# Kernel tuning notes

Measured on AMD Instinct MI355X. Metric: run time of the kernel, lower is better.

The kernel has to match this reference:

```python
import jax, jax.numpy as jnp
import numpy as np

TEMPERATURE = 0.2
HYPER_GAMMA = 0.5
EPS = 1e-12  # torch F.normalize / cosine_similarity eps guard (1e-12 / 1e-8)

def setup_inputs() -> dict:
    key = jax.random.key(0)
    k1, k2 = jax.random.split(key)
    B, D = 4096, 1024
    return {
        "emb_i": jax.random.normal(k1, (B, D), dtype=jnp.float32),
        "emb_j": jax.random.normal(k2, (B, D), dtype=jnp.float32),
    }

def _l2_normalize(x, eps=EPS):
    n = jnp.sqrt(jnp.sum(x * x, axis=1, keepdims=True))
    return x / jnp.maximum(n, eps)

def reference(emb_i, emb_j):
    B = emb_i.shape[0]
    z_i = _l2_normalize(emb_i)
    z_j = _l2_normalize(emb_j)
    # cosine similarity of unit vectors == dot product; sim[a, b] = <z_j[a], z_i[b]>
    sim = jnp.einsum('ad,bd->ab', z_j, z_i)  # [B, B]
    sim_positive = jnp.diagonal(sim)
    positives_exp = jnp.exp(-sim_positive + TEMPERATURE)
    neg_mask = 1.0 - jnp.eye(B, dtype=sim.dtype)
    negatives_exp = neg_mask * jnp.exp(sim - TEMPERATURE)
    positives_sum = jnp.sum(jnp.log1p(positives_exp)) / B
    negatives_sum = jnp.sum(jnp.log1p(negatives_exp)) / (B * (B - 1))
    return HYPER_GAMMA * positives_sum + (1.0 - HYPER_GAMMA) * negatives_sum
```

## Files before the change

kernel.cpp:

```cpp
#include <hip/hip_runtime.h>
#include <math.h>

#define B_ROWS 4096
#define D_DIM  1024
static constexpr float TEMP = 0.2f;
static constexpr float FP8_SCALE = 16.0f;
static constexpr float INV_S2 = 1.0f / 256.0f;

typedef __attribute__((ext_vector_type(4))) float f32x4;

__device__ inline unsigned char f2fp8(float f) {
    unsigned int u = __float_as_uint(f);
    unsigned int s = (u >> 24) & 0x80u;
    float af = fabsf(f);
    unsigned char b;
    if (af >= 0x1.0p-6f) {
        unsigned int au = u & 0x7fffffffu;
        unsigned int lsb = (au >> 20) & 1u;
        au += 0x7ffffu + lsb;
        int e = (int)(au >> 23) - 127 + 7;
        unsigned int m = (au >> 20) & 7u;
        if (e > 15 || (e == 15 && m > 6)) b = 0x7e;
        else b = (unsigned char)((e << 3) | m);
    } else {
        int q = (int)rintf(af * 512.0f);
        b = (unsigned char)(q >= 8 ? 0x08 : q);
    }
    return (unsigned char)(b | s);
}

__device__ inline unsigned int f2fp8x4(float4 v) {
    return (unsigned int)f2fp8(v.x)
         | ((unsigned int)f2fp8(v.y) << 8)
         | ((unsigned int)f2fp8(v.z) << 16)
         | ((unsigned int)f2fp8(v.w) << 24);
}

__device__ inline void gload_lds16(const unsigned char* g, unsigned char* l) {
    __builtin_amdgcn_global_load_lds(
        (const __attribute__((address_space(1))) unsigned int*)g,
        (__attribute__((address_space(3))) unsigned int*)l,
        16, 0, 0);
}


__global__ __launch_bounds__(256) void norm_cast_kernel(
        const float* __restrict__ emb_i, const float* __restrict__ emb_j,
        unsigned char* __restrict__ Zi8, unsigned char* __restrict__ Zj8,
        float* __restrict__ w) {
    const int tid = threadIdx.x;
    if (blockIdx.x == 0 && tid == 0) {
        w[0] = 0.0f; w[1] = 0.0f;
        ((unsigned int*)w)[2] = 0u;
    }
    const int wave = tid >> 6, lane = tid & 63;
    const int row = blockIdx.x * 4 + wave;
    const float* src; unsigned char* dst; int r;
    if (row < B_ROWS) { src = emb_i; dst = Zi8; r = row; }
    else              { src = emb_j; dst = Zj8; r = row - B_ROWS; }

    const float4* p = (const float4*)(src + (size_t)r * D_DIM);
    float4 v0 = p[lane], v1 = p[64 + lane], v2 = p[128 + lane], v3 = p[192 + lane];
    float s = v0.x*v0.x + v0.y*v0.y + v0.z*v0.z + v0.w*v0.w
            + v1.x*v1.x + v1.y*v1.y + v1.z*v1.z + v1.w*v1.w
            + v2.x*v2.x + v2.y*v2.y + v2.z*v2.z + v2.w*v2.w
            + v3.x*v3.x + v3.y*v3.y + v3.z*v3.z + v3.w*v3.w;
    #pragma unroll
    for (int m = 1; m < 64; m <<= 1) s += __shfl_xor(s, m, 64);
    const float inv = FP8_SCALE / fmaxf(sqrtf(s), 1e-12f);

    float4 a0 = {v0.x*inv, v0.y*inv, v0.z*inv, v0.w*inv};
    float4 a1 = {v1.x*inv, v1.y*inv, v1.z*inv, v1.w*inv};
    float4 a2 = {v2.x*inv, v2.y*inv, v2.z*inv, v2.w*inv};
    float4 a3 = {v3.x*inv, v3.y*inv, v3.z*inv, v3.w*inv};
    unsigned int* q = (unsigned int*)(dst + (size_t)r * D_DIM);
    q[lane]       = f2fp8x4(a0);
    q[64 + lane]  = f2fp8x4(a1);
    q[128 + lane] = f2fp8x4(a2);
    q[192 + lane] = f2fp8x4(a3);
}

__global__ __launch_bounds__(256, 2) void simloss_mfma_fp8_kernel(
        const unsigned char* __restrict__ Zi8,
        const unsigned char* __restrict__ Zj8,
        float* __restrict__ w, float* __restrict__ out) {
    __shared__ __align__(16) unsigned char lA[128 * 64];
    __shared__ __align__(16) unsigned char lB[256 * 64];
    __shared__ float rn[4], rp[4];

    const int tid  = threadIdx.x;
    const int lane = tid & 63;
    const int wave = tid >> 6;
    const int wy = wave >> 1, wx = wave & 1;
    const int rowBase = blockIdx.y * 128;
    const int colBase = blockIdx.x * 256;

    const int lrow = lane >> 2;
    const int lp   = lane & 3;
    const int lc   = (lp - (lrow >> 2)) & 3;
    const unsigned char* gA0 = Zj8 + (size_t)(rowBase + (2*wave+0)*16 + lrow) * D_DIM + lc*16;
    const unsigned char* gA1 = Zj8 + (size_t)(rowBase + (2*wave+1)*16 + lrow) * D_DIM + lc*16;
    const unsigned char* gB0 = Zi8 + (size_t)(colBase + (4*wave+0)*16 + lrow) * D_DIM + lc*16;
    const unsigned char* gB1 = Zi8 + (size_t)(colBase + (4*wave+1)*16 + lrow) * D_DIM + lc*16;
    const unsigned char* gB2 = Zi8 + (size_t)(colBase + (4*wave+2)*16 + lrow) * D_DIM + lc*16;
    const unsigned char* gB3 = Zi8 + (size_t)(colBase + (4*wave+3)*16 + lrow) * D_DIM + lc*16;
    unsigned char* sA0 = lA + (2*wave+0) * 1024;
    unsigned char* sA1 = lA + (2*wave+1) * 1024;
    unsigned char* sB0 = lB + (4*wave+0) * 1024;
    unsigned char* sB1 = lB + (4*wave+1) * 1024;
    unsigned char* sB2 = lB + (4*wave+2) * 1024;
    unsigned char* sB3 = lB + (4*wave+3) * 1024;

    const int fr = lane & 15;
    const int q4 = lane >> 4;
    const int qh = q4 >> 1, qb = q4 & 1;
    const int P0 = (qh + 0 + (fr >> 2)) & 3;
    const int P1 = (qh + 2 + (fr >> 2)) & 3;
    const unsigned char* fA0 = lA + (wy * 64 + fr) * 64 + P0 * 16 + qb * 8;
    const unsigned char* fA1 = lA + (wy * 64 + fr) * 64 + P1 * 16 + qb * 8;
    const unsigned char* fB0 = lB + (wx * 128 + fr) * 64 + P0 * 16 + qb * 8;
    const unsigned char* fB1 = lB + (wx * 128 + fr) * 64 + P1 * 16 + qb * 8;

    f32x4 acc[4][8];
    #pragma unroll
    for (int i = 0; i < 4; ++i)
        #pragma unroll
        for (int j = 0; j < 8; ++j)
            acc[i][j] = (f32x4){0.f, 0.f, 0.f, 0.f};

    for (int k0 = 0; k0 < D_DIM; k0 += 64) {
        __syncthreads();
        gload_lds16(gA0, sA0); gload_lds16(gA1, sA1);
        gload_lds16(gB0, sB0); gload_lds16(gB1, sB1);
        gload_lds16(gB2, sB2); gload_lds16(gB3, sB3);
        gA0 += 64; gA1 += 64; gB0 += 64; gB1 += 64; gB2 += 64; gB3 += 64;
        __syncthreads();

        {
            long a[4], b[8];
            #pragma unroll
            for (int i = 0; i < 4; ++i) a[i] = *(const long*)(fA0 + i * 1024);
            #pragma unroll
            for (int j = 0; j < 8; ++j) b[j] = *(const long*)(fB0 + j * 1024);
            #pragma unroll
            for (int i = 0; i < 4; ++i)
                #pragma unroll
                for (int j = 0; j < 8; ++j)
                    acc[i][j] = __builtin_amdgcn_mfma_f32_16x16x32_fp8_fp8(
                        a[i], b[j], acc[i][j], 0, 0, 0);
        }
        {
            long a[4], b[8];
            #pragma unroll
            for (int i = 0; i < 4; ++i) a[i] = *(const long*)(fA1 + i * 1024);
            #pragma unroll
            for (int j = 0; j < 8; ++j) b[j] = *(const long*)(fB1 + j * 1024);
            #pragma unroll
            for (int i = 0; i < 4; ++i)
                #pragma unroll
                for (int j = 0; j < 8; ++j)
                    acc[i][j] = __builtin_amdgcn_mfma_f32_16x16x32_fp8_fp8(
                        a[i], b[j], acc[i][j], 0, 0, 0);
        }
    }

    const int cr = q4 * 4;
    const int cc = lane & 15;
    float neg = 0.f, pos = 0.f;
    #pragma unroll
    for (int i = 0; i < 4; ++i) {
        const int abase = rowBase + wy * 64 + i * 16 + cr;
        #pragma unroll
        for (int j = 0; j < 8; ++j) {
            const int b = colBase + wx * 128 + j * 16 + cc;
            #pragma unroll
            for (int r = 0; r < 4; ++r) {
                const float x = acc[i][j][r] * INV_S2 - TEMP;
                if (abase + r == b) pos += __logf(1.0f + __expf(-x));
                else                neg += __logf(1.0f + __expf(x));
            }
        }
    }
    #pragma unroll
    for (int off = 32; off > 0; off >>= 1) {
        neg += __shfl_down(neg, off, 64);
        pos += __shfl_down(pos, off, 64);
    }
    if (lane == 0) { rn[wave] = neg; rp[wave] = pos; }
    __syncthreads();
    if (tid == 0) {
        atomicAdd(&w[1], rn[0] + rn[1] + rn[2] + rn[3]);
        if ((int)blockIdx.x == (int)(blockIdx.y >> 1))
            atomicAdd(&w[0], rp[0] + rp[1] + rp[2] + rp[3]);
        __threadfence();
        unsigned int done = atomicAdd(((unsigned int*)w) + 2, 1u);
        if (done == gridDim.x * gridDim.y - 1) {
            const float psum = atomicAdd(&w[0], 0.0f);
            const float nsum = atomicAdd(&w[1], 0.0f);
            out[0] = 0.5f * (psum / (float)B_ROWS)
                   + 0.5f * (nsum / ((float)B_ROWS * (float)(B_ROWS - 1)));
        }
    }
}

extern "C" void kernel_launch(void* const* d_in, const int* in_sizes, int n_in,
                              void* d_out, int out_size, void* d_ws, size_t ws_size,
                              hipStream_t stream) {
    const float* emb_i = (const float*)d_in[0];
    const float* emb_j = (const float*)d_in[1];
    float* w = (float*)d_ws;
    unsigned char* Zi8 = (unsigned char*)(w + 16);
    unsigned char* Zj8 = Zi8 + (size_t)B_ROWS * D_DIM;
    float* out = (float*)d_out;

    norm_cast_kernel<<<2 * B_ROWS / 4, 256, 0, stream>>>(emb_i, emb_j, Zi8, Zj8, w);
    dim3 grid(B_ROWS / 256, B_ROWS / 128);
    simloss_mfma_fp8_kernel<<<grid, 256, 0, stream>>>(Zi8, Zj8, w, out);
}
```

Baseline: 118.3 us.

## Switch GEMM to MX-scaled 32x32x64 FP8 MFMA with K=128 tiles and prefetch

Replaces the 16x16x32 FP8 MFMA with the gfx950 scaled 32x32x64 f8f6f4 MFMA, using unit scales, which offers higher peak FP8 throughput. The K tile grows from 64 to 128 bytes per row with a new XOR swizzle. The next stage's global-to-LDS load is issued after the second half's fragments are read into registers, partly overlapping loads with MFMAs. LDS use doubles to 48KB per block, which may limit occupancy, and the epilogue index mapping changes to the 32x32 accumulator layout.

```diff
diff --git a/kernel.cpp b/kernel.cpp
--- a/kernel.cpp
+++ b/kernel.cpp
@@ -7,7 +7,9 @@
 static constexpr float FP8_SCALE = 16.0f;
 static constexpr float INV_S2 = 1.0f / 256.0f;
 
-typedef __attribute__((ext_vector_type(4))) float f32x4;
+typedef __attribute__((ext_vector_type(4)))  int   i32x4;
+typedef __attribute__((ext_vector_type(8)))  int   i32x8;
+typedef __attribute__((ext_vector_type(16))) float f32x16;
 
 __device__ inline unsigned char f2fp8(float f) {
     unsigned int u = __float_as_uint(f);
@@ -43,6 +45,15 @@
         16, 0, 0);
 }
 
+__device__ inline i32x8 read_frag(const unsigned char* p, int o0, int o1) {
+    i32x4 lo = *(const i32x4*)(p + o0);
+    i32x4 hi = *(const i32x4*)(p + o1);
+    return __builtin_shufflevector(lo, hi, 0, 1, 2, 3, 4, 5, 6, 7);
+}
+
+#define MX_MFMA(A, Bv, C) __builtin_amdgcn_mfma_scale_f32_32x32x64_f8f6f4( \
+    (A), (Bv), (C), 0, 0, 0, 0x7f7f7f7f, 0, 0x7f7f7f7f)
+
 
 __global__ __launch_bounds__(256) void norm_cast_kernel(
         const float* __restrict__ emb_i, const float* __restrict__ emb_j,
@@ -80,12 +91,12 @@
     q[192 + lane] = f2fp8x4(a3);
 }
 
-__global__ __launch_bounds__(256, 2) void simloss_mfma_fp8_kernel(
+__global__ __launch_bounds__(256, 2) void simloss_mfma_mxfp8_kernel(
         const unsigned char* __restrict__ Zi8,
         const unsigned char* __restrict__ Zj8,
         float* __restrict__ w, float* __restrict__ out) {
-    __shared__ __align__(16) unsigned char lA[128 * 64];
-    __shared__ __align__(16) unsigned char lB[256 * 64];
+    __shared__ __align__(16) unsigned char lA[128 * 128];
+    __shared__ __align__(16) unsigned char lB[256 * 128];
     __shared__ float rn[4], rp[4];
 
     const int tid  = threadIdx.x;
@@ -95,96 +106,101 @@
     const int rowBase = blockIdx.y * 128;
     const int colBase = blockIdx.x * 256;
 
-    const int lrow = lane >> 2;
-    const int lp   = lane & 3;
-    const int lc   = (lp - (lrow >> 2)) & 3;
-    const unsigned char* gA0 = Zj8 + (size_t)(rowBase + (2*wave+0)*16 + lrow) * D_DIM + lc*16;
-    const unsigned char* gA1 = Zj8 + (size_t)(rowBase + (2*wave+1)*16 + lrow) * D_DIM + lc*16;
-    const unsigned char* gB0 = Zi8 + (size_t)(colBase + (4*wave+0)*16 + lrow) * D_DIM + lc*16;
-    const unsigned char* gB1 = Zi8 + (size_t)(colBase + (4*wave+1)*16 + lrow) * D_DIM + lc*16;
-    const unsigned char* gB2 = Zi8 + (size_t)(colBase + (4*wave+2)*16 + lrow) * D_DIM + lc*16;
-    const unsigned char* gB3 = Zi8 + (size_t)(colBase + (4*wave+3)*16 + lrow) * D_DIM + lc*16;
-    unsigned char* sA0 = lA + (2*wave+0) * 1024;
-    unsigned char* sA1 = lA + (2*wave+1) * 1024;
-    unsigned char* sB0 = lB + (4*wave+0) * 1024;
-    unsigned char* sB1 = lB + (4*wave+1) * 1024;
-    unsigned char* sB2 = lB + (4*wave+2) * 1024;
-    unsigned char* sB3 = lB + (4*wave+3) * 1024;
-
-    const int fr = lane & 15;
-    const int q4 = lane >> 4;
-    const int qh = q4 >> 1, qb = q4 & 1;
-    const int P0 = (qh + 0 + (fr >> 2)) & 3;
-    const int P1 = (qh + 2 + (fr >> 2)) & 3;
-    const unsigned char* fA0 = lA + (wy * 64 + fr) * 64 + P0 * 16 + qb * 8;
-    const unsigned char* fA1 = lA + (wy * 64 + fr) * 64 + P1 * 16 + qb * 8;
-    const unsigned char* fB0 = lB + (wx * 128 + fr) * 64 + P0 * 16 + qb * 8;
-    const unsigned char* fB1 = lB + (wx * 128 + fr) * 64 + P1 * 16 + qb * 8;
-
-    f32x4 acc[4][8];
-    #pragma unroll
-    for (int i = 0; i < 4; ++i)
+    const int srow = lane >> 3;
+    const int sc   = (lane & 7) ^ (srow & 7);
+    const unsigned char* gA = Zj8 + (size_t)(rowBase + 32*wave + srow) * D_DIM + sc*16;
+    const unsigned char* gB = Zi8 + (size_t)(colBase + 64*wave + srow) * D_DIM + sc*16;
+    unsigned char* sA = lA + wave * 4096;
+    unsigned char* sB = lB + wave * 8192;
+
+#define STAGE(k0) do {                                                        \
+        _Pragma("unroll")                                                     \
+        for (int n = 0; n < 4; ++n)                                           \
+            gload_lds16(gA + (size_t)(n*8) * D_DIM + (k0), sA + n*1024);      \
+        _Pragma("unroll")                                                     \
+        for (int n = 0; n < 8; ++n)                                           \
+            gload_lds16(gB + (size_t)(n*8) * D_DIM + (k0), sB + n*1024);      \
+    } while (0)
+
+    const int lr = lane & 31;
+    const int kh = lane >> 5;
+    int off[2][2];
+    #pragma unroll
+    for (int kk = 0; kk < 2; ++kk)
         #pragma unroll
-        for (int j = 0; j < 8; ++j)
-            acc[i][j] = (f32x4){0.f, 0.f, 0.f, 0.f};
-
-    for (int k0 = 0; k0 < D_DIM; k0 += 64) {
+        for (int t = 0; t < 2; ++t)
+            off[kk][t] = ((((kk << 2) + (kh << 1) + t) ^ (lane & 7)) << 4);
+    const unsigned char* fA = lA + (wy * 64  + lr) * 128;
+    const unsigned char* fB = lB + (wx * 128 + lr) * 128;
+
+    f32x16 acc[2][4];
+    #pragma unroll
+    for (int i = 0; i < 2; ++i)
+        #pragma unroll
+        for (int j = 0; j < 4; ++j)
+            #pragma unroll
+            for (int r = 0; r < 16; ++r)
+                acc[i][j][r] = 0.0f;
+
+    STAGE(0);
+    __syncthreads();
+
+    for (int it = 0; it < 8; ++it) {
+        i32x8 a0 = read_frag(fA,         off[0][0], off[0][1]);
+        i32x8 a1 = read_frag(fA + 4096,  off[0][0], off[0][1]);
+        i32x8 b0 = read_frag(fB,         off[0][0], off[0][1]);
+        i32x8 b1 = read_frag(fB + 4096,  off[0][0], off[0][1]);
+        i32x8 b2 = read_frag(fB + 8192,  off[0][0], off[0][1]);
+        i32x8 b3 = read_frag(fB + 12288, off[0][0], off[0][1]);
+        acc[0][0] = MX_MFMA(a0, b0, acc[0][0]);
+        acc[0][1] = MX_MFMA(a0, b1, acc[0][1]);
+        acc[0][2] = MX_MFMA(a0, b2, acc[0][2]);
+        acc[0][3] = MX_MFMA(a0, b3, acc[0][3]);
+        acc[1][0] = MX_MFMA(a1, b0, acc[1][0]);
+        acc[1][1] = MX_MFMA(a1, b1, acc[1][1]);
+        acc[1][2] = MX_MFMA(a1, b2, acc[1][2]);
+        acc[1][3] = MX_MFMA(a1, b3, acc[1][3]);
+        a0 = read_frag(fA,         off[1][0], off[1][1]);
+        a1 = read_frag(fA + 4096,  off[1][0], off[1][1]);
+        b0 = read_frag(fB,         off[1][0], off[1][1]);
+        b1 = read_frag(fB + 4096,  off[1][0], off[1][1]);
+        b2 = read_frag(fB + 8192,  off[1][0], off[1][1]);
+        b3 = read_frag(fB + 12288, off[1][0], off[1][1]);
         __syncthreads();
-        gload_lds16(gA0, sA0); gload_lds16(gA1, sA1);
-        gload_lds16(gB0, sB0); gload_lds16(gB1, sB1);
-        gload_lds16(gB2, sB2); gload_lds16(gB3, sB3);
-        gA0 += 64; gA1 += 64; gB0 += 64; gB1 += 64; gB2 += 64; gB3 += 64;
+        if (it < 7) STAGE((it + 1) * 128);
+        acc[0][0] = MX_MFMA(a0, b0, acc[0][0]);
+        acc[0][1] = MX_MFMA(a0, b1, acc[0][1]);
+        acc[0][2] = MX_MFMA(a0, b2, acc[0][2]);
+        acc[0][3] = MX_MFMA(a0, b3, acc[0][3]);
+        acc[1][0] = MX_MFMA(a1, b0, acc[1][0]);
+        acc[1][1] = MX_MFMA(a1, b1, acc[1][1]);
+        acc[1][2] = MX_MFMA(a1, b2, acc[1][2]);
+        acc[1][3] = MX_MFMA(a1, b3, acc[1][3]);
         __syncthreads();
-
-        {
-            long a[4], b[8];
+    }
+#undef STAGE
+
+    float neg = 0.f, pos = 0.f;
+    const int bc = colBase + wx * 128 + (lane & 31);
+    #pragma unroll
+    for (int i = 0; i < 2; ++i) {
+        const int abase = rowBase + wy * 64 + i * 32 + 4 * kh;
+        #pragma unroll
+        for (int j = 0; j < 4; ++j) {
+            const int b = bc + j * 32;
             #pragma unroll
-            for (int i = 0; i < 4; ++i) a[i] = *(const long*)(fA0 + i * 1024);
-            #pragma unroll
-            for (int j = 0; j < 8; ++j) b[j] = *(const long*)(fB0 + j * 1024);
-            #pragma unroll
-            for (int i = 0; i < 4; ++i)
-                #pragma unroll
-                for (int j = 0; j < 8; ++j)
-                    acc[i][j] = __builtin_amdgcn_mfma_f32_16x16x32_fp8_fp8(
-                        a[i], b[j], acc[i][j], 0, 0, 0);
-        }
-        {
-            long a[4], b[8];
-            #pragma unroll
-            for (int i = 0; i < 4; ++i) a[i] = *(const long*)(fA1 + i * 1024);
-            #pragma unroll
-            for (int j = 0; j < 8; ++j) b[j] = *(const long*)(fB1 + j * 1024);
-            #pragma unroll
-            for (int i = 0; i < 4; ++i)
-                #pragma unroll
-                for (int j = 0; j < 8; ++j)
-                    acc[i][j] = __builtin_amdgcn_mfma_f32_16x16x32_fp8_fp8(
-                        a[i], b[j], acc[i][j], 0, 0, 0);
-        }
-    }
-
-    const int cr = q4 * 4;
-    const int cc = lane & 15;
-    float neg = 0.f, pos = 0.f;
-    #pragma unroll
-    for (int i = 0; i < 4; ++i) {
-        const int abase = rowBase + wy * 64 + i * 16 + cr;
-        #pragma unroll
-        for (int j = 0; j < 8; ++j) {
-            const int b = colBase + wx * 128 + j * 16 + cc;
-            #pragma unroll
-            for (int r = 0; r < 4; ++r) {
+            for (int r = 0; r < 16; ++r) {
+                const int arow = abase + (r & 3) + 8 * (r >> 2);
                 const float x = acc[i][j][r] * INV_S2 - TEMP;
-                if (abase + r == b) pos += __logf(1.0f + __expf(-x));
-                else                neg += __logf(1.0f + __expf(x));
+                if (arow == b) pos += __logf(1.0f + __expf(-x));
+                else           neg += __logf(1.0f + __expf(x));
             }
         }
     }
     #pragma unroll
-    for (int off = 32; off > 0; off >>= 1) {
-        neg += __shfl_down(neg, off, 64);
-        pos += __shfl_down(pos, off, 64);
+    for (int o = 32; o > 0; o >>= 1) {
+        neg += __shfl_down(neg, o, 64);
+        pos += __shfl_down(pos, o, 64);
     }
     if (lane == 0) { rn[wave] = neg; rp[wave] = pos; }
     __syncthreads();
@@ -215,5 +231,5 @@
 
     norm_cast_kernel<<<2 * B_ROWS / 4, 256, 0, stream>>>(emb_i, emb_j, Zi8, Zj8, w);
     dim3 grid(B_ROWS / 256, B_ROWS / 128);
-    simloss_mfma_fp8_kernel<<<grid, 256, 0, stream>>>(Zi8, Zj8, w, out);
-}
+    simloss_mfma_mxfp8_kernel<<<grid, 256, 0, stream>>>(Zi8, Zj8, w, out);
+}
```

New measurement: 279.1 us. 2.36x slower.
